# Kernel optimization log

Measured on AMD Instinct MI355X. Metric: run time of the kernel, lower is better.

## Reference

```python
import jax, jax.numpy as jnp
import numpy as np

FRAMES, RANK = 128, 5          # rank=5 implied by create_adj6 non_adj index lists (max index 4)
N = FRAMES * RANK              # 640 nodes
B, NFEAT, NHID, NCLASS = 128, 256, 8, 16
ALPHA = 0.2                    # LeakyReLU negative slope
MASK_VAL = -9e15               # hard mask value from the torch code


def create_adj6(frames, rank):
    """Block-diagonal (with holes) + chain adjacency, exactly as in the torch source."""
    adj = np.zeros((frames * rank, frames * rank), dtype=np.float32)
    non_adj_x = [0, 0, 1, 2, 3, 3, 4, 4]
    non_adj_y = [3, 4, 4, 3, 0, 2, 0, 1]
    for i in range(frames):
        adj[rank * i:rank * (i + 1), rank * i:rank * (i + 1)] = 1
        for j in range(len(non_adj_x)):
            adj[rank * i + non_adj_x[j], rank * i + non_adj_y[j]] = 0
        for j in range(rank):
            if i > 0:
                adj[rank * i + j, rank * (i - 1) + j] = 1
            if i < frames - 1:
                adj[rank * i + j, rank * (i + 1) + j] = 1
    return adj


def _xavier(key, shape):
    fan_in, fan_out = shape[0], shape[1]
    std = np.sqrt(2.0) * np.sqrt(2.0 / (fan_in + fan_out))  # gain=sqrt(2) xavier_normal
    return std * jax.random.normal(key, shape, dtype=jnp.float32)


def setup_inputs() -> dict:
    key = jax.random.key(0)
    ks = jax.random.split(key, 7)
    x = jax.random.normal(ks[0], (B, N, NFEAT), dtype=jnp.float32)
    W1 = _xavier(ks[1], (NFEAT, NHID))
    a11 = _xavier(ks[2], (NHID, 1))
    a12 = _xavier(ks[3], (NHID, 1))
    W2 = _xavier(ks[4], (NHID, NCLASS))  # nhid*nheads=8 -> nclass=16
    a21 = _xavier(ks[5], (NCLASS, 1))
    a22 = _xavier(ks[6], (NCLASS, 1))
    adj = jnp.asarray(create_adj6(FRAMES, RANK) > 0)  # bool [N, N]
    return dict(x=x, W1=W1, a11=a11, a12=a12, W2=W2, a21=a21, a22=a22, adj=adj)


def gat_layer(xi, adj, W, a1, a2):
    # xi: [N, F_in]
    h = xi @ W                              # [N, F_out]
    f1 = h @ a1                             # [N, 1]
    f2 = h @ a2                             # [N, 1]
    e = jax.nn.leaky_relu(f1 + f2.T, negative_slope=ALPHA)  # [N, N]
    scores = jnp.where(adj, e, jnp.float32(MASK_VAL))        # hard additive-style mask
    att = jax.nn.softmax(scores, axis=-1)   # dropout disabled (eval mode)
    return att @ h                          # [N, F_out]


def reference(x, W1, a11, a12, W2, a21, a22, adj):
    def single(xi):
        h1 = gat_layer(xi, adj, W1, a11, a12)          # concat=False -> no elu inside layer
        h2 = jax.nn.elu(gat_layer(h1, adj, W2, a21, a22))
        return jax.nn.log_softmax(h2, axis=1)          # [N, NCLASS]
    return jax.vmap(single)(x)                          # [B, N, NCLASS]
```

## Files before the change

### kernel.cpp

```cpp
#include <hip/hip_runtime.h>
#include <stdint.h>

#define B_ 128
#define N_ 640
#define NFEAT 256
#define NHID 8
#define NCLASS 16
#define RANK 5
#define FRAMES 128
#define ALPHA 0.2f
#define PACKMASK 30236135u

typedef short bf16x8 __attribute__((ext_vector_type(8)));
typedef float f32x4  __attribute__((ext_vector_type(4)));
typedef unsigned int u32x4 __attribute__((ext_vector_type(4)));

#define GA_ROWS 64
#define GA_GRID (B_ * N_ / GA_ROWS)

__device__ __forceinline__ void cvt8(float4 p, float4 q, bf16x8& hi, bf16x8& lo)
{
    float v[8] = {p.x, p.y, p.z, p.w, q.x, q.y, q.z, q.w};
    u32x4 hw, lw;
#pragma unroll
    for (int i = 0; i < 4; ++i) {
        const unsigned ua = __float_as_uint(v[2 * i]);
        const unsigned ub = __float_as_uint(v[2 * i + 1]);
        hw[i] = (ua >> 16) | (ub & 0xFFFF0000u);
        const float la = v[2 * i]     - __uint_as_float(ua & 0xFFFF0000u);
        const float lb = v[2 * i + 1] - __uint_as_float(ub & 0xFFFF0000u);
        const unsigned va = __float_as_uint(la), vb = __float_as_uint(lb);
        lw[i] = ((va + 0x7FFFu + ((va >> 16) & 1u)) >> 16)
              | ((vb + 0x7FFFu + ((vb >> 16) & 1u)) & 0xFFFF0000u);
    }
    hi = __builtin_bit_cast(bf16x8, hw);
    lo = __builtin_bit_cast(bf16x8, lw);
}

__global__ void __launch_bounds__(256) k_gemm(
    const float* __restrict__ x, const float* __restrict__ W1,
    float* __restrict__ h1ws)
{
    const int tid = threadIdx.x;
    const int w   = tid >> 6;
    const int l   = tid & 63;
    const int rowbase = blockIdx.x * GA_ROWS;

    const int n  = l & 15;
    const int kg = (l >> 4) << 3;

    const float* xrow = x + (size_t)(rowbase + w * 16 + n) * NFEAT + kg;
    float4 xv[16];
#pragma unroll
    for (int ks = 0; ks < 8; ++ks) {
        xv[2 * ks]     = *reinterpret_cast<const float4*>(xrow + ks * 32);
        xv[2 * ks + 1] = *reinterpret_cast<const float4*>(xrow + ks * 32 + 4);
    }

    bf16x8 bhi[8], blo[8];
#pragma unroll
    for (int ks = 0; ks < 8; ++ks) {
        u32x4 hw, lw;
#pragma unroll
        for (int p = 0; p < 4; ++p) {
            float wa = 0.0f, wb = 0.0f;
            if (n < NHID) {
                const int k0 = ks * 32 + kg + 2 * p;
                wa = W1[k0 * NHID + n];
                wb = W1[(k0 + 1) * NHID + n];
            }
            const unsigned ua = __float_as_uint(wa), ub = __float_as_uint(wb);
            hw[p] = (ua >> 16) | (ub & 0xFFFF0000u);
            const float la = wa - __uint_as_float(ua & 0xFFFF0000u);
            const float lb = wb - __uint_as_float(ub & 0xFFFF0000u);
            const unsigned va = __float_as_uint(la), vb = __float_as_uint(lb);
            lw[p] = ((va + 0x7FFFu + ((va >> 16) & 1u)) >> 16)
                  | ((vb + 0x7FFFu + ((vb >> 16) & 1u)) & 0xFFFF0000u);
        }
        bhi[ks] = __builtin_bit_cast(bf16x8, hw);
        blo[ks] = __builtin_bit_cast(bf16x8, lw);
    }

    f32x4 acc = {0.f, 0.f, 0.f, 0.f};
#pragma unroll
    for (int ks = 0; ks < 8; ++ks) {
        bf16x8 ahi, alo;
        cvt8(xv[2 * ks], xv[2 * ks + 1], ahi, alo);
        acc = __builtin_amdgcn_mfma_f32_16x16x32_bf16(ahi, bhi[ks], acc, 0, 0, 0);
        acc = __builtin_amdgcn_mfma_f32_16x16x32_bf16(alo, bhi[ks], acc, 0, 0, 0);
        acc = __builtin_amdgcn_mfma_f32_16x16x32_bf16(ahi, blo[ks], acc, 0, 0, 0);
    }

    if (n < NHID) {
        float* hp = h1ws + ((size_t)rowbase + w * 16 + (l >> 4) * 4) * NHID + n;
#pragma unroll
        for (int j = 0; j < 4; ++j) hp[j * NHID] = acc[j];
    }
}

#define QSPLIT 16
#define TFRAMES (FRAMES / QSPLIT)
#define TCOUNT (TFRAMES * RANK)
#define BLOCKB 64
#define MAXSTAGE 60
#define H1S 9
#define H2S 17

#define OFF_F1S (MAXSTAGE * H1S)
#define OFF_F2S (OFF_F1S + MAXSTAGE)
#define OFF_G1S (MAXSTAGE * H2S)
#define OFF_G2S (OFF_G1S + MAXSTAGE)
#define SMEMF (OFF_G2S + MAXSTAGE)

__device__ __forceinline__ float lrelu(float v) { return v >= 0.0f ? v : ALPHA * v; }

__global__ void __launch_bounds__(BLOCKB, 8) k_attn(
    const float* __restrict__ h1ws,
    const float* __restrict__ a11, const float* __restrict__ a12,
    const float* __restrict__ W2, const float* __restrict__ a21, const float* __restrict__ a22,
    float* __restrict__ out)
{
    __shared__ float smem[SMEMF];
    float* h1s = smem;
    float* f1s = smem + OFF_F1S;
    float* f2s = smem + OFF_F2S;
    float* h2s = smem;
    float* g1s = smem + OFF_G1S;
    float* g2s = smem + OFF_G2S;

    const int bid = blockIdx.x;
    const int bq  = (bid & 7) * 256 + (bid >> 3);
    const int b   = bq >> 4;
    const int q   = bq & 15;

    const int tf_lo  = q * TFRAMES;
    const int l1f_lo = max(tf_lo - 1, 0);
    const int l1f_hi = min(tf_lo + TFRAMES, FRAMES - 1);
    const int stf_lo = max(tf_lo - 2, 0);
    const int stf_hi = min(tf_lo + TFRAMES + 1, FRAMES - 1);
    const int stage_lo  = stf_lo * RANK;
    const int stage_cnt = (stf_hi - stf_lo + 1) * RANK;
    const int l1_lo  = l1f_lo * RANK;
    const int l1_cnt = (l1f_hi - l1f_lo + 1) * RANK;
    const int t_lo   = tf_lo * RANK;

    const int tid = threadIdx.x;

    if (tid < stage_cnt) {
        const float* hp = h1ws + ((size_t)b * N_ + stage_lo + tid) * NHID;
        const float4 p = *reinterpret_cast<const float4*>(hp);
        const float4 q4 = *reinterpret_cast<const float4*>(hp + 4);
        float hv[NHID] = {p.x, p.y, p.z, p.w, q4.x, q4.y, q4.z, q4.w};
        float s1 = 0.0f, s2 = 0.0f;
#pragma unroll
        for (int k = 0; k < NHID; ++k) {
            s1 = fmaf(hv[k], a11[k], s1);
            s2 = fmaf(hv[k], a12[k], s2);
            h1s[tid * H1S + k] = hv[k];
        }
        f1s[tid] = s1;
        f2s[tid] = s2;
    }
    __syncthreads();

    float h2[NCLASS];
    float s1g = 0.0f, s2g = 0.0f;
    const bool actL1 = (tid < l1_cnt);
    if (actL1) {
        const int u  = l1_lo + tid;
        const int fr = u / RANK;
        const int ru = u - fr * RANK;
        const unsigned rm = (PACKMASK >> (5 * ru)) & 31u;
        const int loc      = u - stage_lo;
        const int base_loc = fr * RANK - stage_lo;
        const bool hp = (fr > 0), hn = (fr < FRAMES - 1);
        const float fu = f1s[loc];

        float m = -1e30f;
        if (hp) m = fmaxf(m, lrelu(fu + f2s[loc - RANK]));
#pragma unroll
        for (int rv = 0; rv < RANK; ++rv)
            if (rm & (1u << rv)) m = fmaxf(m, lrelu(fu + f2s[base_loc + rv]));
        if (hn) m = fmaxf(m, lrelu(fu + f2s[loc + RANK]));

        float s = 0.0f;
        float o1[NHID];
#pragma unroll
        for (int k = 0; k < NHID; ++k) o1[k] = 0.0f;

        auto acc1 = [&](int vloc) {
            float w = __expf(lrelu(fu + f2s[vloc]) - m);
            s += w;
#pragma unroll
            for (int k = 0; k < NHID; ++k) o1[k] = fmaf(w, h1s[vloc * H1S + k], o1[k]);
        };
        if (hp) acc1(loc - RANK);
#pragma unroll
        for (int rv = 0; rv < RANK; ++rv)
            if (rm & (1u << rv)) acc1(base_loc + rv);
        if (hn) acc1(loc + RANK);

        const float inv = 1.0f / s;
#pragma unroll
        for (int k = 0; k < NHID; ++k) o1[k] *= inv;

#pragma unroll
        for (int c = 0; c < NCLASS; ++c) {
            float t = 0.0f;
#pragma unroll
            for (int k = 0; k < NHID; ++k) t = fmaf(o1[k], W2[k * NCLASS + c], t);
            h2[c] = t;
            s1g = fmaf(t, a21[c], s1g);
            s2g = fmaf(t, a22[c], s2g);
        }
    }
    __syncthreads();

    if (actL1) {
        const int loc = l1_lo + tid - stage_lo;
#pragma unroll
        for (int c = 0; c < NCLASS; ++c) h2s[loc * H2S + c] = h2[c];
        g1s[loc] = s1g;
        g2s[loc] = s2g;
    }
    __syncthreads();

    if (tid < TCOUNT) {
        const int u  = t_lo + tid;
        const int fr = u / RANK;
        const int ru = u - fr * RANK;
        const unsigned rm = (PACKMASK >> (5 * ru)) & 31u;
        const int loc      = u - stage_lo;
        const int base_loc = fr * RANK - stage_lo;
        const bool hp = (fr > 0), hn = (fr < FRAMES - 1);
        const float gu = g1s[loc];

        float m = -1e30f;
        if (hp) m = fmaxf(m, lrelu(gu + g2s[loc - RANK]));
#pragma unroll
        for (int rv = 0; rv < RANK; ++rv)
            if (rm & (1u << rv)) m = fmaxf(m, lrelu(gu + g2s[base_loc + rv]));
        if (hn) m = fmaxf(m, lrelu(gu + g2s[loc + RANK]));

        float s = 0.0f;
        float o2[NCLASS];
#pragma unroll
        for (int c = 0; c < NCLASS; ++c) o2[c] = 0.0f;

        auto acc2 = [&](int vloc) {
            float w = __expf(lrelu(gu + g2s[vloc]) - m);
            s += w;
#pragma unroll
            for (int c = 0; c < NCLASS; ++c) o2[c] = fmaf(w, h2s[vloc * H2S + c], o2[c]);
        };
        if (hp) acc2(loc - RANK);
#pragma unroll
        for (int rv = 0; rv < RANK; ++rv)
            if (rm & (1u << rv)) acc2(base_loc + rv);
        if (hn) acc2(loc + RANK);

        const float inv = 1.0f / s;
#pragma unroll
        for (int c = 0; c < NCLASS; ++c) o2[c] *= inv;

#pragma unroll
        for (int c = 0; c < NCLASS; ++c) o2[c] = (o2[c] > 0.0f) ? o2[c] : __expf(o2[c]) - 1.0f;

        float mm = o2[0];
#pragma unroll
        for (int c = 1; c < NCLASS; ++c) mm = fmaxf(mm, o2[c]);
        float ss = 0.0f;
#pragma unroll
        for (int c = 0; c < NCLASS; ++c) ss += __expf(o2[c] - mm);
        const float ls = mm + __logf(ss);

        float* op = out + ((size_t)b * N_ + u) * NCLASS;
#pragma unroll
        for (int c = 0; c < NCLASS; c += 4)
            *reinterpret_cast<float4*>(op + c) =
                make_float4(o2[c] - ls, o2[c + 1] - ls, o2[c + 2] - ls, o2[c + 3] - ls);
    }
}

extern "C" void kernel_launch(void* const* d_in, const int* in_sizes, int n_in,
                              void* d_out, int out_size, void* d_ws, size_t ws_size,
                              hipStream_t stream)
{
    const float* x   = (const float*)d_in[0];
    const float* W1  = (const float*)d_in[1];
    const float* a11 = (const float*)d_in[2];
    const float* a12 = (const float*)d_in[3];
    const float* W2  = (const float*)d_in[4];
    const float* a21 = (const float*)d_in[5];
    const float* a22 = (const float*)d_in[6];
    float* outp  = (float*)d_out;
    float* h1ws  = (float*)d_ws;

    k_gemm<<<GA_GRID, 256, 0, stream>>>(x, W1, h1ws);
    k_attn<<<B_ * QSPLIT, BLOCKB, 0, stream>>>(h1ws, a11, a12, W2, a21, a22, outp);
}
```

Before: 32.58 us.

## Fuse projection GEMM into attention kernel with halo recompute per block

Merges the x@W1 MFMA projection into the attention kernel. Each block computes h1 for its frame range plus a two-frame halo directly into shared memory, and the block count drops to four per batch with 384 threads. This removes the h1 workspace round trip through global memory and the second kernel launch. In exchange, halo rows of x are read and projected twice (about an eighth extra traffic). Holding two row tiles per wave also raises register use.

```diff
diff --git a/kernel.cpp b/kernel.cpp
--- a/kernel.cpp
+++ b/kernel.cpp
@@ -11,12 +11,25 @@
 #define ALPHA 0.2f
 #define PACKMASK 30236135u
 
+#define QSPLIT 4
+#define TFRAMES (FRAMES / QSPLIT)
+#define TCOUNT (TFRAMES * RANK)
+#define BLOCKT 384
+#define MAXSTAGE 180
+#define H1S 9
+#define H2S 17
+
+#define OFF_F1S (MAXSTAGE * H1S)
+#define OFF_F2S (OFF_F1S + MAXSTAGE)
+#define OFF_G1S (MAXSTAGE * H2S)
+#define OFF_G2S (OFF_G1S + MAXSTAGE)
+#define SMEMF (OFF_G2S + MAXSTAGE)
+
 typedef short bf16x8 __attribute__((ext_vector_type(8)));
 typedef float f32x4  __attribute__((ext_vector_type(4)));
 typedef unsigned int u32x4 __attribute__((ext_vector_type(4)));
 
-#define GA_ROWS 64
-#define GA_GRID (B_ * N_ / GA_ROWS)
+__device__ __forceinline__ float lrelu(float v) { return v >= 0.0f ? v : ALPHA * v; }
 
 __device__ __forceinline__ void cvt8(float4 p, float4 q, bf16x8& hi, bf16x8& lo)
 {
@@ -37,24 +50,53 @@
     lo = __builtin_bit_cast(bf16x8, lw);
 }
 
-__global__ void __launch_bounds__(256) k_gemm(
+__global__ void __launch_bounds__(BLOCKT, 2) k_fused(
     const float* __restrict__ x, const float* __restrict__ W1,
-    float* __restrict__ h1ws)
+    const float* __restrict__ a11, const float* __restrict__ a12,
+    const float* __restrict__ W2, const float* __restrict__ a21, const float* __restrict__ a22,
+    float* __restrict__ out)
 {
+    __shared__ float smem[SMEMF];
+    float* h1s = smem;
+    float* f1s = smem + OFF_F1S;
+    float* f2s = smem + OFF_F2S;
+    float* h2s = smem;
+    float* g1s = smem + OFF_G1S;
+    float* g2s = smem + OFF_G2S;
+
+    const int bid = blockIdx.x;
+    const int bq  = (bid & 7) * 64 + (bid >> 3);
+    const int b   = bq >> 2;
+    const int q   = bq & 3;
+
+    const int tf_lo  = q * TFRAMES;
+    const int l1f_lo = max(tf_lo - 1, 0);
+    const int l1f_hi = min(tf_lo + TFRAMES, FRAMES - 1);
+    const int stf_lo = max(tf_lo - 2, 0);
+    const int stf_hi = min(tf_lo + TFRAMES + 1, FRAMES - 1);
+    const int stage_lo  = stf_lo * RANK;
+    const int stage_cnt = (stf_hi - stf_lo + 1) * RANK;
+    const int l1_lo  = l1f_lo * RANK;
+    const int l1_cnt = (l1f_hi - l1f_lo + 1) * RANK;
+    const int t_lo   = tf_lo * RANK;
+
     const int tid = threadIdx.x;
     const int w   = tid >> 6;
     const int l   = tid & 63;
-    const int rowbase = blockIdx.x * GA_ROWS;
-
-    const int n  = l & 15;
-    const int kg = (l >> 4) << 3;
-
-    const float* xrow = x + (size_t)(rowbase + w * 16 + n) * NFEAT + kg;
-    float4 xv[16];
-#pragma unroll
-    for (int ks = 0; ks < 8; ++ks) {
-        xv[2 * ks]     = *reinterpret_cast<const float4*>(xrow + ks * 32);
-        xv[2 * ks + 1] = *reinterpret_cast<const float4*>(xrow + ks * 32 + 4);
+    const int n   = l & 15;
+    const int kq  = l >> 4;
+    const int kg  = kq << 3;
+
+
+    const int r0  = min(32 * w + n, stage_cnt - 1);
+    const int r1  = min(32 * w + 16 + n, stage_cnt - 1);
+    const float* x0 = x + ((size_t)b * N_ + stage_lo + r0) * NFEAT + kg;
+    const float* x1 = x + ((size_t)b * N_ + stage_lo + r1) * NFEAT + kg;
+    float4 xv0[16];
+#pragma unroll
+    for (int ks = 0; ks < 8; ++ks) {
+        xv0[2 * ks]     = *reinterpret_cast<const float4*>(x0 + ks * 32);
+        xv0[2 * ks + 1] = *reinterpret_cast<const float4*>(x0 + ks * 32 + 4);
     }
 
     bf16x8 bhi[8], blo[8];
@@ -81,82 +123,49 @@
         blo[ks] = __builtin_bit_cast(bf16x8, lw);
     }
 
-    f32x4 acc = {0.f, 0.f, 0.f, 0.f};
+    float4 xv1[16];
+#pragma unroll
+    for (int ks = 0; ks < 8; ++ks) {
+        xv1[2 * ks]     = *reinterpret_cast<const float4*>(x1 + ks * 32);
+        xv1[2 * ks + 1] = *reinterpret_cast<const float4*>(x1 + ks * 32 + 4);
+    }
+
+    f32x4 acc0 = {0.f, 0.f, 0.f, 0.f}, acc1 = {0.f, 0.f, 0.f, 0.f};
 #pragma unroll
     for (int ks = 0; ks < 8; ++ks) {
         bf16x8 ahi, alo;
-        cvt8(xv[2 * ks], xv[2 * ks + 1], ahi, alo);
-        acc = __builtin_amdgcn_mfma_f32_16x16x32_bf16(ahi, bhi[ks], acc, 0, 0, 0);
-        acc = __builtin_amdgcn_mfma_f32_16x16x32_bf16(alo, bhi[ks], acc, 0, 0, 0);
-        acc = __builtin_amdgcn_mfma_f32_16x16x32_bf16(ahi, blo[ks], acc, 0, 0, 0);
+        cvt8(xv0[2 * ks], xv0[2 * ks + 1], ahi, alo);
+        acc0 = __builtin_amdgcn_mfma_f32_16x16x32_bf16(ahi, bhi[ks], acc0, 0, 0, 0);
+        acc0 = __builtin_amdgcn_mfma_f32_16x16x32_bf16(alo, bhi[ks], acc0, 0, 0, 0);
+        acc0 = __builtin_amdgcn_mfma_f32_16x16x32_bf16(ahi, blo[ks], acc0, 0, 0, 0);
+    }
+#pragma unroll
+    for (int ks = 0; ks < 8; ++ks) {
+        bf16x8 ahi, alo;
+        cvt8(xv1[2 * ks], xv1[2 * ks + 1], ahi, alo);
+        acc1 = __builtin_amdgcn_mfma_f32_16x16x32_bf16(ahi, bhi[ks], acc1, 0, 0, 0);
+        acc1 = __builtin_amdgcn_mfma_f32_16x16x32_bf16(alo, bhi[ks], acc1, 0, 0, 0);
+        acc1 = __builtin_amdgcn_mfma_f32_16x16x32_bf16(ahi, blo[ks], acc1, 0, 0, 0);
     }
 
     if (n < NHID) {
-        float* hp = h1ws + ((size_t)rowbase + w * 16 + (l >> 4) * 4) * NHID + n;
-#pragma unroll
-        for (int j = 0; j < 4; ++j) hp[j * NHID] = acc[j];
-    }
-}
-
-#define QSPLIT 16
-#define TFRAMES (FRAMES / QSPLIT)
-#define TCOUNT (TFRAMES * RANK)
-#define BLOCKB 64
-#define MAXSTAGE 60
-#define H1S 9
-#define H2S 17
-
-#define OFF_F1S (MAXSTAGE * H1S)
-#define OFF_F2S (OFF_F1S + MAXSTAGE)
-#define OFF_G1S (MAXSTAGE * H2S)
-#define OFF_G2S (OFF_G1S + MAXSTAGE)
-#define SMEMF (OFF_G2S + MAXSTAGE)
-
-__device__ __forceinline__ float lrelu(float v) { return v >= 0.0f ? v : ALPHA * v; }
-
-__global__ void __launch_bounds__(BLOCKB, 8) k_attn(
-    const float* __restrict__ h1ws,
-    const float* __restrict__ a11, const float* __restrict__ a12,
-    const float* __restrict__ W2, const float* __restrict__ a21, const float* __restrict__ a22,
-    float* __restrict__ out)
-{
-    __shared__ float smem[SMEMF];
-    float* h1s = smem;
-    float* f1s = smem + OFF_F1S;
-    float* f2s = smem + OFF_F2S;
-    float* h2s = smem;
-    float* g1s = smem + OFF_G1S;
-    float* g2s = smem + OFF_G2S;
-
-    const int bid = blockIdx.x;
-    const int bq  = (bid & 7) * 256 + (bid >> 3);
-    const int b   = bq >> 4;
-    const int q   = bq & 15;
-
-    const int tf_lo  = q * TFRAMES;
-    const int l1f_lo = max(tf_lo - 1, 0);
-    const int l1f_hi = min(tf_lo + TFRAMES, FRAMES - 1);
-    const int stf_lo = max(tf_lo - 2, 0);
-    const int stf_hi = min(tf_lo + TFRAMES + 1, FRAMES - 1);
-    const int stage_lo  = stf_lo * RANK;
-    const int stage_cnt = (stf_hi - stf_lo + 1) * RANK;
-    const int l1_lo  = l1f_lo * RANK;
-    const int l1_cnt = (l1f_hi - l1f_lo + 1) * RANK;
-    const int t_lo   = tf_lo * RANK;
-
-    const int tid = threadIdx.x;
+#pragma unroll
+        for (int j = 0; j < 4; ++j) {
+            const int rr0 = 32 * w + kq * 4 + j;
+            if (rr0 < stage_cnt) h1s[rr0 * H1S + n] = acc0[j];
+            const int rr1 = 32 * w + 16 + kq * 4 + j;
+            if (rr1 < stage_cnt) h1s[rr1 * H1S + n] = acc1[j];
+        }
+    }
+    __syncthreads();
 
     if (tid < stage_cnt) {
-        const float* hp = h1ws + ((size_t)b * N_ + stage_lo + tid) * NHID;
-        const float4 p = *reinterpret_cast<const float4*>(hp);
-        const float4 q4 = *reinterpret_cast<const float4*>(hp + 4);
-        float hv[NHID] = {p.x, p.y, p.z, p.w, q4.x, q4.y, q4.z, q4.w};
         float s1 = 0.0f, s2 = 0.0f;
 #pragma unroll
         for (int k = 0; k < NHID; ++k) {
-            s1 = fmaf(hv[k], a11[k], s1);
-            s2 = fmaf(hv[k], a12[k], s2);
-            h1s[tid * H1S + k] = hv[k];
+            const float v = h1s[tid * H1S + k];
+            s1 = fmaf(v, a11[k], s1);
+            s2 = fmaf(v, a12[k], s2);
         }
         f1s[tid] = s1;
         f2s[tid] = s2;
@@ -188,17 +197,17 @@
 #pragma unroll
         for (int k = 0; k < NHID; ++k) o1[k] = 0.0f;
 
-        auto acc1 = [&](int vloc) {
-            float w = __expf(lrelu(fu + f2s[vloc]) - m);
-            s += w;
-#pragma unroll
-            for (int k = 0; k < NHID; ++k) o1[k] = fmaf(w, h1s[vloc * H1S + k], o1[k]);
+        auto acc1f = [&](int vloc) {
+            float wgt = __expf(lrelu(fu + f2s[vloc]) - m);
+            s += wgt;
+#pragma unroll
+            for (int k = 0; k < NHID; ++k) o1[k] = fmaf(wgt, h1s[vloc * H1S + k], o1[k]);
         };
-        if (hp) acc1(loc - RANK);
+        if (hp) acc1f(loc - RANK);
 #pragma unroll
         for (int rv = 0; rv < RANK; ++rv)
-            if (rm & (1u << rv)) acc1(base_loc + rv);
-        if (hn) acc1(loc + RANK);
+            if (rm & (1u << rv)) acc1f(base_loc + rv);
+        if (hn) acc1f(loc + RANK);
 
         const float inv = 1.0f / s;
 #pragma unroll
@@ -247,17 +256,17 @@
 #pragma unroll
         for (int c = 0; c < NCLASS; ++c) o2[c] = 0.0f;
 
-        auto acc2 = [&](int vloc) {
-            float w = __expf(lrelu(gu + g2s[vloc]) - m);
-            s += w;
-#pragma unroll
-            for (int c = 0; c < NCLASS; ++c) o2[c] = fmaf(w, h2s[vloc * H2S + c], o2[c]);
+        auto acc2f = [&](int vloc) {
+            float wgt = __expf(lrelu(gu + g2s[vloc]) - m);
+            s += wgt;
+#pragma unroll
+            for (int c = 0; c < NCLASS; ++c) o2[c] = fmaf(wgt, h2s[vloc * H2S + c], o2[c]);
         };
-        if (hp) acc2(loc - RANK);
+        if (hp) acc2f(loc - RANK);
 #pragma unroll
         for (int rv = 0; rv < RANK; ++rv)
-            if (rm & (1u << rv)) acc2(base_loc + rv);
-        if (hn) acc2(loc + RANK);
+            if (rm & (1u << rv)) acc2f(base_loc + rv);
+        if (hn) acc2f(loc + RANK);
 
         const float inv = 1.0f / s;
 #pragma unroll
@@ -293,9 +302,7 @@
     const float* W2  = (const float*)d_in[4];
     const float* a21 = (const float*)d_in[5];
     const float* a22 = (const float*)d_in[6];
-    float* outp  = (float*)d_out;
-    float* h1ws  = (float*)d_ws;
-
-    k_gemm<<<GA_GRID, 256, 0, stream>>>(x, W1, h1ws);
-    k_attn<<<B_ * QSPLIT, BLOCKB, 0, stream>>>(h1ws, a11, a12, W2, a21, a22, outp);
+    float* outp = (float*)d_out;
+
+    k_fused<<<B_ * QSPLIT, BLOCKT, 0, stream>>>(x, W1, a11, a12, W2, a21, a22, outp);
 }
```

After: 36.40 us. 1.12x slower.
